# Kernel optimization log

Measured on AMD Instinct MI355X. Metric: run time of the kernel, lower is better.

Reference implementation:

```python
import jax, jax.numpy as jnp
import numpy as np

B, T, DMODEL = 2, 2048, 1024
H, DK, DV = 16, 64, 64
FF = 4096
EPS = 1e-5


def _layernorm_2d(x):
    # torch LayerNorm(normalized_shape=(T, dmodel)): normalize jointly over last two
    # dims, biased variance, weight=1 / bias=0 (freshly constructed each forward).
    mu = jnp.mean(x, axis=(1, 2), keepdims=True)
    var = jnp.mean((x - mu) ** 2, axis=(1, 2), keepdims=True)
    return (x - mu) / jnp.sqrt(var + EPS)


def setup_inputs() -> dict:
    key = jax.random.key(0)
    ks = jax.random.split(key, 9)
    s = 0.02  # small init for numerical sanity (original uses uniform(-1,1))
    return {
        "x": jax.random.normal(ks[0], (B, T, DMODEL), jnp.float32),
        "Wq": jax.random.normal(ks[1], (H, DMODEL, DK), jnp.float32) * s,
        "Wk": jax.random.normal(ks[2], (H, DMODEL, DK), jnp.float32) * s,
        "Wv": jax.random.normal(ks[3], (H, DMODEL, DV), jnp.float32) * s,
        "Wo": jax.random.normal(ks[4], (DMODEL, DMODEL), jnp.float32) * s,
        "W1": jax.random.normal(ks[5], (DMODEL, FF), jnp.float32) * s,
        "b1": jnp.zeros((FF,), jnp.float32),
        "W2": jax.random.normal(ks[6], (FF, DMODEL), jnp.float32) * s,
        "b2": jnp.zeros((DMODEL,), jnp.float32),
    }


def reference(x, Wq, Wk, Wv, Wo, W1, b1, W2, b2):
    b, t, d = x.shape
    h, _, dk = Wq.shape
    dv = Wv.shape[-1]
    # per-head projections: (B,H,T,dk/dv)
    Qp = jnp.einsum("btd,hdk->bhtk", x, Wq)
    Kp = jnp.einsum("btd,hdk->bhtk", x, Wk)
    Vp = jnp.einsum("btd,hdv->bhtv", x, Wv)
    scores = jnp.einsum("bhqk,bhsk->bhqs", Qp, Kp) / np.sqrt(dk).astype(np.float32)
    # NOTE: original does torch.softmax(heads, 2) -> softmax over the QUERY axis
    attn = jax.nn.softmax(scores, axis=2)
    heads = jnp.einsum("bhqs,bhsv->bqhv", attn, Vp).reshape(b, t, h * dv)
    att_out = heads @ Wo
    o1 = _layernorm_2d(x + att_out)
    ff = jnp.maximum(o1 @ W1 + b1, 0.0) @ W2 + b2
    return _layernorm_2d(o1 + ff)
```

## Files before the change

kernel.cpp:

```cpp
#include <hip/hip_runtime.h>
#include <hip/hip_bf16.h>
#include <cstddef>
#include <cstdint>

typedef __hip_bfloat16 hbf;
typedef __attribute__((ext_vector_type(8))) __bf16 bf16x8;
typedef __attribute__((ext_vector_type(4))) float f32x4;

#define B_ 2
#define T_ 2048
#define D_ 1024
#define H_ 16
#define FF_ 4096
#define EPS_ 1e-5f
#define SCALE_ 0.125f

__device__ __forceinline__ float bf2f(hbf v) { return __bfloat162float(v); }
__device__ __forceinline__ float ldin(const void* p, size_t i, int isbf) {
  return isbf ? __bfloat162float(((const hbf*)p)[i]) : ((const float*)p)[i];
}
__device__ __forceinline__ void ston(void* p, size_t i, float v, int isbf) {
  if (isbf) ((hbf*)p)[i] = __float2bfloat16(v);
  else ((float*)p)[i] = v;
}
__device__ __forceinline__ f32x4 mfma16(bf16x8 a, bf16x8 b, f32x4 c) {
  return __builtin_amdgcn_mfma_f32_16x16x32_bf16(a, b, c, 0, 0, 0);
}
__device__ __forceinline__ bf16x8 ldfrag(const hbf* p) {
  return *(const bf16x8*)p;
}
__device__ __forceinline__ void glds16(const hbf* g, hbf* l) {
  __builtin_amdgcn_global_load_lds(
      (const __attribute__((address_space(1))) void*)g,
      (__attribute__((address_space(3))) void*)l, 16, 0, 0);
}

__global__ __launch_bounds__(256) void detect_dtype(const unsigned* x,
                                                    int* flag) {
  __shared__ int cnt[256];
  int c = 0;
  for (int i = threadIdx.x; i < 4096; i += 256) {
    unsigned low = x[i] & 0xFFFFu;
    unsigned e = (low >> 7) & 0xFFu;
    if (e >= 100u && e <= 142u) c++;
  }
  cnt[threadIdx.x] = c;
  __syncthreads();
  for (int off = 128; off > 0; off >>= 1) {
    if ((int)threadIdx.x < off) cnt[threadIdx.x] += cnt[threadIdx.x + off];
    __syncthreads();
  }
  if (threadIdx.x == 0) *flag = (cnt[0] > 2458) ? 1 : 0;
}

__device__ __forceinline__ void tr_tile(const void* __restrict__ src,
                                        hbf* __restrict__ dst, int R, int C,
                                        size_t zoff, int cx, int ry, int f,
                                        float (*tile)[33]) {
  const int tx = threadIdx.x & 31, ty = threadIdx.x >> 5;
  const int c0 = cx * 32, r0 = ry * 32;
#pragma unroll
  for (int p = 0; p < 4; p++) {
    int rr = p * 8 + ty;
    tile[rr][tx] = ldin(src, zoff + (size_t)(r0 + rr) * C + c0 + tx, f);
  }
  __syncthreads();
#pragma unroll
  for (int p = 0; p < 4; p++) {
    int cc = p * 8 + ty;
    dst[zoff + (size_t)(c0 + cc) * R + r0 + tx] = __float2bfloat16(tile[tx][cc]);
  }
}

__global__ __launch_bounds__(256) void preconv(
    const void* __restrict__ x, const void* __restrict__ Wq,
    const void* __restrict__ Wk, const void* __restrict__ Wv,
    const void* __restrict__ Wo, const void* __restrict__ W1,
    const void* __restrict__ W2, const void* __restrict__ b1,
    const void* __restrict__ b2, hbf* __restrict__ xb,
    hbf* __restrict__ wqkvt, hbf* __restrict__ wot, hbf* __restrict__ w1t,
    hbf* __restrict__ w2t, hbf* __restrict__ b1b, hbf* __restrict__ b2b,
    const int* __restrict__ flag) {
  __shared__ float tile[32][33];
  const int f = *flag;
  const int bid = blockIdx.x;
  if (bid < 3072) {
    int which = bid >> 10;
    int r = bid & 1023;
    int z = r >> 6, rem = r & 63;
    int ry = rem >> 1, cx = rem & 1;
    const void* src = (which == 0) ? Wq : (which == 1) ? Wk : Wv;
    hbf* dst = wqkvt + (size_t)which * (D_ * D_);
    tr_tile(src, dst, 1024, 64, (size_t)z * 65536, cx, ry, f, tile);
  } else if (bid < 4096) {
    int t = bid - 3072;
    tr_tile(Wo, wot, 1024, 1024, 0, t & 31, t >> 5, f, tile);
  } else if (bid < 8192) {
    int t = bid - 4096;
    tr_tile(W1, w1t, 1024, 4096, 0, t & 127, t >> 7, f, tile);
  } else if (bid < 12288) {
    int t = bid - 8192;
    tr_tile(W2, w2t, 4096, 1024, 0, t & 31, t >> 5, f, tile);
  } else if (bid < 13312) {
    size_t base = (size_t)(bid - 12288) * 4096;
    for (int i = threadIdx.x; i < 4096; i += 256)
      xb[base + i] = __float2bfloat16(ldin(x, base + i, f));
  } else if (bid == 13312) {
    for (int i = threadIdx.x; i < FF_; i += 256)
      b1b[i] = __float2bfloat16(ldin(b1, i, f));
  } else {
    for (int i = threadIdx.x; i < D_; i += 256)
      b2b[i] = __float2bfloat16(ldin(b2, i, f));
  }
}

template <int MODE, int BM, int BN>
__global__ __launch_bounds__(256) void gemm_bt(
    const hbf* __restrict__ A, const hbf* __restrict__ Bt, hbf* __restrict__ C,
    float* __restrict__ Cf0, float* __restrict__ Cf1,
    const hbf* __restrict__ e1, float* __restrict__ red, int M, int N, int K,
    int LDK) {
  constexpr int WM = BM / 2, WN = BN / 2;
  constexpr int IF = WM / 16, JF = WN / 16;
  __shared__ alignas(16) hbf As[BM * 64];
  __shared__ alignas(16) hbf Bs[BN * 64];
  const int tid = threadIdx.x;
  const int wave = tid >> 6, lane = tid & 63;
  const int quad = lane >> 4, l16 = lane & 15;
  const int m0 = blockIdx.y * BM, n0 = blockIdx.x * BN;
  const int mw = (wave >> 1) * WM, nw = (wave & 1) * WN;
  const int srow = tid >> 3;
  const int scol = (tid & 7) * 8;
  const int kbase = (MODE == 4) ? blockIdx.z * K : 0;
  const f32x4 zero = {0.f, 0.f, 0.f, 0.f};
  f32x4 acc[IF][JF];
#pragma unroll
  for (int i = 0; i < IF; i++)
#pragma unroll
    for (int j = 0; j < JF; j++) acc[i][j] = zero;

  const hbf* ga = &A[(size_t)(m0 + srow) * LDK + kbase + scol];
  const hbf* gb = &Bt[(size_t)(n0 + srow) * LDK + kbase + scol];
  hbf* lA = &As[wave * 512];
  hbf* lB = &Bs[wave * 512];

  for (int k0 = 0; k0 < K; k0 += 64) {
#pragma unroll
    for (int c = 0; c < BM / 32; c++)
      glds16(ga + (size_t)(c * 32) * LDK + k0, lA + c * 2048);
#pragma unroll
    for (int c = 0; c < BN / 32; c++)
      glds16(gb + (size_t)(c * 32) * LDK + k0, lB + c * 2048);
    __syncthreads();
    bf16x8 af[2][IF], bfr[2][JF];
#pragma unroll
    for (int h = 0; h < 2; h++) {
#pragma unroll
      for (int i = 0; i < IF; i++)
        af[h][i] = ldfrag(&As[(mw + i * 16 + l16) * 64 + h * 32 + quad * 8]);
#pragma unroll
      for (int j = 0; j < JF; j++)
        bfr[h][j] = ldfrag(&Bs[(nw + j * 16 + l16) * 64 + h * 32 + quad * 8]);
    }
#pragma unroll
    for (int h = 0; h < 2; h++)
#pragma unroll
      for (int i = 0; i < IF; i++)
#pragma unroll
        for (int j = 0; j < JF; j++)
          acc[i][j] = mfma16(af[h][i], bfr[h][j], acc[i][j]);
    __syncthreads();
  }
  float ssum = 0.f, ssq = 0.f;
#pragma unroll
  for (int i = 0; i < IF; i++)
#pragma unroll
    for (int j = 0; j < JF; j++)
#pragma unroll
      for (int r = 0; r < 4; r++) {
        int m = m0 + mw + i * 16 + quad * 4 + r;
        int n = n0 + nw + j * 16 + l16;
        float v = acc[i][j][r];
        if (MODE == 0) {
          int which = n >> 10, n1 = n & 1023;
          int h = n1 >> 6, cc = n1 & 63;
          int b = m >> 11, t = m & (T_ - 1);
          if (which == 0) v *= SCALE_;
          C[(size_t)which * ((size_t)B_ * H_ * T_ * 64) +
            (((size_t)(b * H_ + h)) * T_ + t) * 64 + cc] = __float2bfloat16(v);
        } else if (MODE == 1) {
          hbf hv = __float2bfloat16(v + bf2f(e1[(size_t)m * N + n]));
          C[(size_t)m * N + n] = hv;
          float fv = bf2f(hv);
          ssum += fv;
          ssq += fv * fv;
        } else if (MODE == 2) {
          C[(size_t)m * N + n] = __float2bfloat16(fmaxf(v + bf2f(e1[n]), 0.f));
        } else if (MODE == 4) {
          float* Cf = blockIdx.z ? Cf1 : Cf0;
          Cf[(size_t)m * N + n] = v;
        }
      }
  if (MODE == 1) {
    float* sc = (float*)As;
    sc[tid] = ssum;
    sc[256 + tid] = ssq;
    __syncthreads();
    for (int off = 128; off > 0; off >>= 1) {
      if (tid < off) {
        sc[tid] += sc[tid + off];
        sc[256 + tid] += sc[256 + tid + off];
      }
      __syncthreads();
    }
    if (tid == 0) {
      int b = m0 >> 11;
      atomicAdd(&red[b * 2 + 0], sc[0]);
      atomicAdd(&red[b * 2 + 1], sc[256]);
    }
  }
}

__global__ __launch_bounds__(256) void attn_stats(const hbf* __restrict__ Q,
                                                  const hbf* __restrict__ K,
                                                  const hbf* __restrict__ V,
                                                  hbf* __restrict__ Vt) {
  __shared__ alignas(16) hbf Ks[64 * 72];
  __shared__ alignas(16) hbf Qs[64 * 72];
  __shared__ float sAdj[64];
  const int bh = blockIdx.y;
  const int s0 = blockIdx.x * 64;
  const int tid = threadIdx.x;
  const int wave = tid >> 6, lane = tid & 63;
  const int quad = lane >> 4, l16 = lane & 15;
  const int sw = wave * 16;
  const hbf* Kb = K + (size_t)bh * T_ * 64;
  const hbf* Qb = Q + (size_t)bh * T_ * 64;
  const hbf* Vb = V + (size_t)bh * T_ * 64;
  hbf* Vtb = Vt + (size_t)bh * 64 * T_;
  const int r_ = tid >> 3, c_ = (tid & 7) * 8;
#pragma unroll
  for (int c = 0; c < 2; c++) {
    int row = c * 32 + r_;
    *(float4*)(&Ks[row * 72 + c_]) =
        *(const float4*)(&Kb[(size_t)(s0 + row) * 64 + c_]);
  }
  __syncthreads();
  bf16x8 kf0 = ldfrag(&Ks[(sw + l16) * 72 + quad * 8]);
  bf16x8 kf1 = ldfrag(&Ks[(sw + l16) * 72 + 32 + quad * 8]);
  float m_thr[4], l_thr[4];
#pragma unroll
  for (int r = 0; r < 4; r++) {
    m_thr[r] = -1e30f;
    l_thr[r] = 0.f;
  }
  const f32x4 zero = {0.f, 0.f, 0.f, 0.f};
  for (int qt = 0; qt < T_ / 64; qt++) {
    if (qt) __syncthreads();
#pragma unroll
    for (int c = 0; c < 2; c++) {
      int row = c * 32 + r_;
      *(float4*)(&Qs[row * 72 + c_]) =
          *(const float4*)(&Qb[(size_t)(qt * 64 + row) * 64 + c_]);
    }
    __syncthreads();
    f32x4 acc[4];
#pragma unroll
    for (int j = 0; j < 4; j++) {
      bf16x8 qf0 = ldfrag(&Qs[(j * 16 + l16) * 72 + quad * 8]);
      bf16x8 qf1 = ldfrag(&Qs[(j * 16 + l16) * 72 + 32 + quad * 8]);
      f32x4 a = zero;
      a = mfma16(kf0, qf0, a);
      a = mfma16(kf1, qf1, a);
      acc[j] = a;
    }
#pragma unroll
    for (int r = 0; r < 4; r++) {
      float mt = fmaxf(fmaxf(acc[0][r], acc[1][r]),
                       fmaxf(acc[2][r], acc[3][r]));
      float nm = fmaxf(m_thr[r], mt);
      float s = l_thr[r] * __expf(m_thr[r] - nm);
#pragma unroll
      for (int j = 0; j < 4; j++) s += __expf(acc[j][r] - nm);
      l_thr[r] = s;
      m_thr[r] = nm;
    }
  }
#pragma unroll
  for (int d = 1; d < 16; d <<= 1) {
#pragma unroll
    for (int r = 0; r < 4; r++) {
      float om = __shfl_xor(m_thr[r], d);
      float ol = __shfl_xor(l_thr[r], d);
      float nm = fmaxf(m_thr[r], om);
      l_thr[r] = l_thr[r] * __expf(m_thr[r] - nm) + ol * __expf(om - nm);
      m_thr[r] = nm;
    }
  }
  if (l16 == 0) {
#pragma unroll
    for (int r = 0; r < 4; r++)
      sAdj[sw + quad * 4 + r] = m_thr[r] + __logf(l_thr[r]);
  }
  __syncthreads();
#pragma unroll
  for (int c = 0; c < 2; c++) {
    int e = (c * 256 + tid) * 8;
    int r = e >> 6, col = e & 63;
    union alignas(16) {
      hbf h[8];
      float4 f4;
    } u;
    u.f4 = *(const float4*)(&Vb[(size_t)(s0 + r) * 64 + col]);
    float sc = __expf(-sAdj[r]);
#pragma unroll
    for (int k2 = 0; k2 < 8; k2++)
      u.h[k2] = __float2bfloat16(bf2f(u.h[k2]) * sc);
    *(float4*)(&Ks[r * 72 + col]) = u.f4;
  }
  __syncthreads();
#pragma unroll
  for (int c = 0; c < 2; c++) {
    int e = (c * 256 + tid) * 8;
    int v = e >> 6, tt = e & 63;
    union alignas(16) {
      hbf h[8];
      float4 f4;
    } u;
#pragma unroll
    for (int k2 = 0; k2 < 8; k2++) u.h[k2] = Ks[(tt + k2) * 72 + v];
    *(float4*)(&Vtb[(size_t)v * T_ + s0 + tt]) = u.f4;
  }
}

__global__ __launch_bounds__(256) void attn_apply(const hbf* __restrict__ Q,
                                                  const hbf* __restrict__ K,
                                                  const hbf* __restrict__ Vt,
                                                  hbf* __restrict__ heads) {
  __shared__ alignas(16) hbf Ks[64 * 72];
  __shared__ alignas(16) hbf Vs[64 * 72];
  __shared__ alignas(16) hbf Ps[4 * 32 * 72];
  const int bh = blockIdx.y;
  const int b = bh >> 4, h = bh & 15;
  const int q0 = blockIdx.x * 128;
  const int tid = threadIdx.x;
  const int wave = tid >> 6, lane = tid & 63;
  const int quad = lane >> 4, l16 = lane & 15;
  const int qw = wave * 32;
  const hbf* Qb = Q + (size_t)bh * T_ * 64;
  const hbf* Kb = K + (size_t)bh * T_ * 64;
  const hbf* Vtb = Vt + (size_t)bh * 64 * T_;
  hbf* Pw = &Ps[wave * 32 * 72];
  const int r_ = tid >> 3, c_ = (tid & 7) * 8;
  bf16x8 qf[2][2];
#pragma unroll
  for (int i = 0; i < 2; i++)
#pragma unroll
    for (int hh = 0; hh < 2; hh++)
      qf[i][hh] = *(const bf16x8*)&Qb[(size_t)(q0 + qw + i * 16 + l16) * 64 +
                                      hh * 32 + quad * 8];
  const f32x4 zero = {0.f, 0.f, 0.f, 0.f};
  f32x4 accO[2][4];
#pragma unroll
  for (int i = 0; i < 2; i++)
#pragma unroll
    for (int j = 0; j < 4; j++) accO[i][j] = zero;

  for (int st = 0; st < T_ / 64; st++) {
    if (st) __syncthreads();
#pragma unroll
    for (int c = 0; c < 2; c++) {
      int row = c * 32 + r_;
      *(float4*)(&Ks[row * 72 + c_]) =
          *(const float4*)(&Kb[(size_t)(st * 64 + row) * 64 + c_]);
      *(float4*)(&Vs[row * 72 + c_]) =
          *(const float4*)(&Vtb[(size_t)row * T_ + st * 64 + c_]);
    }
    __syncthreads();
    f32x4 accS[2][4];
#pragma unroll
    for (int j = 0; j < 4; j++) {
      bf16x8 kf0 = ldfrag(&Ks[(j * 16 + l16) * 72 + quad * 8]);
      bf16x8 kf1 = ldfrag(&Ks[(j * 16 + l16) * 72 + 32 + quad * 8]);
#pragma unroll
      for (int i = 0; i < 2; i++) {
        f32x4 a = zero;
        a = mfma16(qf[i][0], kf0, a);
        a = mfma16(qf[i][1], kf1, a);
        accS[i][j] = a;
      }
    }
#pragma unroll
    for (int j = 0; j < 4; j++) {
#pragma unroll
      for (int i = 0; i < 2; i++)
#pragma unroll
        for (int r = 0; r < 4; r++) {
          float p = __expf(accS[i][j][r]);
          Pw[(i * 16 + quad * 4 + r) * 72 + j * 16 + l16] =
              __float2bfloat16(p);
        }
    }
    bf16x8 pf[2][2];
#pragma unroll
    for (int i = 0; i < 2; i++) {
      pf[i][0] = ldfrag(&Pw[(i * 16 + l16) * 72 + quad * 8]);
      pf[i][1] = ldfrag(&Pw[(i * 16 + l16) * 72 + 32 + quad * 8]);
    }
#pragma unroll
    for (int j2 = 0; j2 < 4; j2++) {
      bf16x8 vf0 = ldfrag(&Vs[(j2 * 16 + l16) * 72 + quad * 8]);
      bf16x8 vf1 = ldfrag(&Vs[(j2 * 16 + l16) * 72 + 32 + quad * 8]);
#pragma unroll
      for (int i = 0; i < 2; i++) {
        accO[i][j2] = mfma16(pf[i][0], vf0, accO[i][j2]);
        accO[i][j2] = mfma16(pf[i][1], vf1, accO[i][j2]);
      }
    }
  }
#pragma unroll
  for (int i = 0; i < 2; i++)
#pragma unroll
    for (int j2 = 0; j2 < 4; j2++)
#pragma unroll
      for (int r = 0; r < 4; r++) {
        int q = q0 + qw + i * 16 + quad * 4 + r;
        int v = j2 * 16 + l16;
        heads[((size_t)(b * T_ + q)) * D_ + h * 64 + v] =
            __float2bfloat16(accO[i][j2][r]);
      }
}

__global__ __launch_bounds__(256) void ln_norm(const hbf* __restrict__ src,
                                               const float* __restrict__ red,
                                               void* dst,
                                               const int* __restrict__ flag,
                                               int force_bf) {
  const int isbf = force_bf ? 1 : *flag;
  const float invN = 1.f / (float)(T_ * D_);
  for (size_t i = (size_t)blockIdx.x * 256 + threadIdx.x;
       i < (size_t)B_ * T_ * D_; i += (size_t)gridDim.x * 256) {
    int b = (int)(i >> 21);
    float mu = red[b * 2 + 0] * invN;
    float var = red[b * 2 + 1] * invN - mu * mu;
    ston(dst, i, (bf2f(src[i]) - mu) * rsqrtf(var + EPS_), isbf);
  }
}

__global__ __launch_bounds__(256) void ln2_stats(const float* __restrict__ P0,
                                                 const float* __restrict__ P1,
                                                 const hbf* __restrict__ o1,
                                                 const hbf* __restrict__ b2b,
                                                 float* __restrict__ red) {
  __shared__ float s1[256], s2[256];
  const int b = blockIdx.y;
  const size_t base = (size_t)b * (T_ * D_);
  float sum = 0.f, sq = 0.f;
  for (size_t i = (size_t)blockIdx.x * 256 + threadIdx.x; i < (size_t)T_ * D_;
       i += (size_t)gridDim.x * 256) {
    size_t e = base + i;
    float v = P0[e] + P1[e] + bf2f(b2b[i & (D_ - 1)]) + bf2f(o1[e]);
    sum += v;
    sq += v * v;
  }
  s1[threadIdx.x] = sum;
  s2[threadIdx.x] = sq;
  __syncthreads();
  for (int off = 128; off > 0; off >>= 1) {
    if ((int)threadIdx.x < off) {
      s1[threadIdx.x] += s1[threadIdx.x + off];
      s2[threadIdx.x] += s2[threadIdx.x + off];
    }
    __syncthreads();
  }
  if (threadIdx.x == 0) {
    atomicAdd(&red[b * 2 + 0], s1[0]);
    atomicAdd(&red[b * 2 + 1], s2[0]);
  }
}

__global__ __launch_bounds__(256) void ln2_norm(
    const float* __restrict__ P0, const float* __restrict__ P1,
    const hbf* __restrict__ o1, const hbf* __restrict__ b2b,
    const float* __restrict__ red, void* dst, const int* __restrict__ flag) {
  const int isbf = *flag;
  const float invN = 1.f / (float)(T_ * D_);
  for (size_t i = (size_t)blockIdx.x * 256 + threadIdx.x;
       i < (size_t)B_ * T_ * D_; i += (size_t)gridDim.x * 256) {
    int b = (int)(i >> 21);
    float mu = red[b * 2 + 0] * invN;
    float var = red[b * 2 + 1] * invN - mu * mu;
    float v = P0[i] + P1[i] + bf2f(b2b[i & (D_ - 1)]) + bf2f(o1[i]);
    ston(dst, i, (v - mu) * rsqrtf(var + EPS_), isbf);
  }
}

extern "C" void kernel_launch(void* const* d_in, const int* in_sizes, int n_in,
                              void* d_out, int out_size, void* d_ws,
                              size_t ws_size, hipStream_t stream) {
  const void* x = d_in[0];
  const void* Wq = d_in[1];
  const void* Wk = d_in[2];
  const void* Wv = d_in[3];
  const void* Wo = d_in[4];
  const void* W1 = d_in[5];
  const void* W2 = d_in[7];
  const void* b1 = d_in[6];
  const void* b2 = d_in[8];

  const size_t MB = 1024 * 1024;
  if (ws_size < 89 * MB) return;

  char* w = (char*)d_ws;
  hbf* xb = (hbf*)(w + 0 * MB);
  hbf* wqkvt = (hbf*)(w + 8 * MB);
  hbf* wot = (hbf*)(w + 14 * MB);
  hbf* w1t = (hbf*)(w + 16 * MB);
  hbf* w2t = (hbf*)(w + 24 * MB);
  hbf* Qb = (hbf*)(w + 32 * MB);
  hbf* Kb = (hbf*)(w + 40 * MB);
  hbf* Vb = (hbf*)(w + 48 * MB);
  hbf* Vtb = (hbf*)(w + 56 * MB);
  hbf* heads = (hbf*)(w + 64 * MB);
  hbf* r1 = (hbf*)(w + 72 * MB);
  hbf* o1 = (hbf*)(w + 80 * MB);
  hbf* ff1 = (hbf*)(w + 32 * MB);
  float* P0 = (float*)(w + 0 * MB);
  float* P1 = (float*)(w + 64 * MB);
  hbf* b1b = (hbf*)(w + 88 * MB);
  hbf* b2b = b1b + FF_;
  float* red = (float*)(b2b + D_);
  int* flag = (int*)(red + 8);

  hipMemsetAsync(red, 0, 8 * sizeof(float) + sizeof(int), stream);
  detect_dtype<<<1, 256, 0, stream>>>((const unsigned*)x, flag);

  const int M = B_ * T_;
  preconv<<<13314, 256, 0, stream>>>(x, Wq, Wk, Wv, Wo, W1, W2, b1, b2, xb,
                                     wqkvt, wot, w1t, w2t, b1b, b2b, flag);
  gemm_bt<0, 128, 128><<<dim3(24, 32), 256, 0, stream>>>(
      xb, wqkvt, Qb, nullptr, nullptr, nullptr, nullptr, M, 3 * D_, D_, D_);
  attn_stats<<<dim3(32, 32), 256, 0, stream>>>(Qb, Kb, Vb, Vtb);
  attn_apply<<<dim3(16, 32), 256, 0, stream>>>(Qb, Kb, Vtb, heads);
  gemm_bt<1, 128, 64><<<dim3(16, 32), 256, 0, stream>>>(
      heads, wot, r1, nullptr, nullptr, xb, red, M, D_, D_, D_);
  ln_norm<<<4096, 256, 0, stream>>>(r1, red, o1, flag, 1);
  gemm_bt<2, 128, 128><<<dim3(32, 32), 256, 0, stream>>>(
      o1, w1t, ff1, nullptr, nullptr, b1b, nullptr, M, FF_, D_, D_);
  gemm_bt<4, 128, 128><<<dim3(8, 32, 2), 256, 0, stream>>>(
      ff1, w2t, nullptr, P0, P1, nullptr, nullptr, M, D_, FF_ / 2, FF_);
  ln2_stats<<<dim3(256, B_), 256, 0, stream>>>(P0, P1, o1, b2b, red + 4);
  ln2_norm<<<2048, 256, 0, stream>>>(P0, P1, o1, b2b, red + 4, d_out, flag);
}
```

Before: 475.7 us.

## Fold LayerNorm1 into FFN1 GEMM, drop max tracking in softmax, prefetch attention tiles

Removes the ln_norm kernel. LayerNorm1 is folded into the W1 GEMM epilogue through the identity (x-mu)*rs@W1 = (x@W1 - mu*colsum(W1))*rs, with W1 column sums precomputed in preconv, and LN2 recomputes o1 from r1. The attention softmax drops the running-max rescaling: Q is pre-scaled by log2(e)/8 and raw exp2 is used, which assumes scores are small enough not to overflow. Attention kernels also prefetch the next Q or K/V tile into registers, and the memset is merged into detect_dtype. The changes trade numerical robustness and extra W1 reads for fewer passes and launches.

After: 611.4 us. 1.29x slower.

```diff
diff --git a/kernel.cpp b/kernel.cpp
--- a/kernel.cpp
+++ b/kernel.cpp
@@ -13,7 +13,7 @@
 #define H_ 16
 #define FF_ 4096
 #define EPS_ 1e-5f
-#define SCALE_ 0.125f
+#define QSCALE_ 0.18033688f
 
 __device__ __forceinline__ float bf2f(hbf v) { return __bfloat162float(v); }
 __device__ __forceinline__ float ldin(const void* p, size_t i, int isbf) {
@@ -28,6 +28,15 @@
 }
 __device__ __forceinline__ bf16x8 ldfrag(const hbf* p) {
   return *(const bf16x8*)p;
+}
+__device__ __forceinline__ float fexp2(float x) {
+#if __has_builtin(__builtin_amdgcn_exp2f)
+  return __builtin_amdgcn_exp2f(x);
+#else
+  float r;
+  asm("v_exp_f32 %0, %1" : "=v"(r) : "v"(x));
+  return r;
+#endif
 }
 __device__ __forceinline__ void glds16(const hbf* g, hbf* l) {
   __builtin_amdgcn_global_load_lds(
@@ -36,8 +45,9 @@
 }
 
 __global__ __launch_bounds__(256) void detect_dtype(const unsigned* x,
-                                                    int* flag) {
+                                                    int* flag, float* red) {
   __shared__ int cnt[256];
+  if (threadIdx.x < 8) red[threadIdx.x] = 0.f;
   int c = 0;
   for (int i = threadIdx.x; i < 4096; i += 256) {
     unsigned low = x[i] & 0xFFFFu;
@@ -80,7 +90,7 @@
     const void* __restrict__ b2, hbf* __restrict__ xb,
     hbf* __restrict__ wqkvt, hbf* __restrict__ wot, hbf* __restrict__ w1t,
     hbf* __restrict__ w2t, hbf* __restrict__ b1b, hbf* __restrict__ b2b,
-    const int* __restrict__ flag) {
+    float* __restrict__ sW1, const int* __restrict__ flag) {
   __shared__ float tile[32][33];
   const int f = *flag;
   const int bid = blockIdx.x;
@@ -108,18 +118,23 @@
   } else if (bid == 13312) {
     for (int i = threadIdx.x; i < FF_; i += 256)
       b1b[i] = __float2bfloat16(ldin(b1, i, f));
-  } else {
+  } else if (bid == 13313) {
     for (int i = threadIdx.x; i < D_; i += 256)
       b2b[i] = __float2bfloat16(ldin(b2, i, f));
+  } else {
+    int n = (bid - 13314) * 256 + threadIdx.x;
+    float s = 0.f;
+    for (int k = 0; k < D_; k++) s += ldin(W1, (size_t)k * FF_ + n, f);
+    sW1[n] = s;
   }
 }
 
 template <int MODE, int BM, int BN>
 __global__ __launch_bounds__(256) void gemm_bt(
     const hbf* __restrict__ A, const hbf* __restrict__ Bt, hbf* __restrict__ C,
-    float* __restrict__ Cf0, float* __restrict__ Cf1,
-    const hbf* __restrict__ e1, float* __restrict__ red, int M, int N, int K,
-    int LDK) {
+    float* __restrict__ Cf0, float* __restrict__ Cf1, float* __restrict__ Cf2,
+    const hbf* __restrict__ e1, float* __restrict__ red,
+    const float* __restrict__ sW1, int M, int N, int K, int LDK) {
   constexpr int WM = BM / 2, WN = BN / 2;
   constexpr int IF = WM / 16, JF = WN / 16;
   __shared__ alignas(16) hbf As[BM * 64];
@@ -171,6 +186,14 @@
           acc[i][j] = mfma16(af[h][i], bfr[h][j], acc[i][j]);
     __syncthreads();
   }
+  float mu = 0.f, rs = 0.f;
+  if (MODE == 5) {
+    const float invN = 1.f / (float)(T_ * D_);
+    int b = m0 >> 11;
+    mu = red[b * 2 + 0] * invN;
+    float var = red[b * 2 + 1] * invN - mu * mu;
+    rs = rsqrtf(var + EPS_);
+  }
   float ssum = 0.f, ssq = 0.f;
 #pragma unroll
   for (int i = 0; i < IF; i++)
@@ -185,7 +208,7 @@
           int which = n >> 10, n1 = n & 1023;
           int h = n1 >> 6, cc = n1 & 63;
           int b = m >> 11, t = m & (T_ - 1);
-          if (which == 0) v *= SCALE_;
+          if (which == 0) v *= QSCALE_;
           C[(size_t)which * ((size_t)B_ * H_ * T_ * 64) +
             (((size_t)(b * H_ + h)) * T_ + t) * 64 + cc] = __float2bfloat16(v);
         } else if (MODE == 1) {
@@ -194,11 +217,16 @@
           float fv = bf2f(hv);
           ssum += fv;
           ssq += fv * fv;
-        } else if (MODE == 2) {
-          C[(size_t)m * N + n] = __float2bfloat16(fmaxf(v + bf2f(e1[n]), 0.f));
         } else if (MODE == 4) {
-          float* Cf = blockIdx.z ? Cf1 : Cf0;
-          Cf[(size_t)m * N + n] = v;
+          if (blockIdx.z == 0) {
+            Cf0[(size_t)m * N + n] = v;
+          } else {
+            float* Cf = (m >> 11) ? Cf2 : Cf1;
+            Cf[(size_t)(m & 2047) * N + n] = v;
+          }
+        } else if (MODE == 5) {
+          float o = (v - mu * sW1[n]) * rs + bf2f(e1[n]);
+          C[(size_t)m * N + n] = __float2bfloat16(fmaxf(o, 0.f));
         }
       }
   if (MODE == 1) {
@@ -227,7 +255,7 @@
                                                   hbf* __restrict__ Vt) {
   __shared__ alignas(16) hbf Ks[64 * 72];
   __shared__ alignas(16) hbf Qs[64 * 72];
-  __shared__ float sAdj[64];
+  __shared__ float sSc[64];
   const int bh = blockIdx.y;
   const int s0 = blockIdx.x * 64;
   const int tid = threadIdx.x;
@@ -245,25 +273,27 @@
     *(float4*)(&Ks[row * 72 + c_]) =
         *(const float4*)(&Kb[(size_t)(s0 + row) * 64 + c_]);
   }
+  float4 qreg[2];
+#pragma unroll
+  for (int c = 0; c < 2; c++)
+    qreg[c] = *(const float4*)(&Qb[(size_t)(c * 32 + r_) * 64 + c_]);
   __syncthreads();
   bf16x8 kf0 = ldfrag(&Ks[(sw + l16) * 72 + quad * 8]);
   bf16x8 kf1 = ldfrag(&Ks[(sw + l16) * 72 + 32 + quad * 8]);
-  float m_thr[4], l_thr[4];
-#pragma unroll
-  for (int r = 0; r < 4; r++) {
-    m_thr[r] = -1e30f;
-    l_thr[r] = 0.f;
-  }
+  float l_thr[4] = {0.f, 0.f, 0.f, 0.f};
   const f32x4 zero = {0.f, 0.f, 0.f, 0.f};
   for (int qt = 0; qt < T_ / 64; qt++) {
-    if (qt) __syncthreads();
-#pragma unroll
-    for (int c = 0; c < 2; c++) {
-      int row = c * 32 + r_;
-      *(float4*)(&Qs[row * 72 + c_]) =
-          *(const float4*)(&Qb[(size_t)(qt * 64 + row) * 64 + c_]);
-    }
-    __syncthreads();
+#pragma unroll
+    for (int c = 0; c < 2; c++)
+      *(float4*)(&Qs[(c * 32 + r_) * 72 + c_]) = qreg[c];
+    __syncthreads();
+    if (qt + 1 < T_ / 64) {
+#pragma unroll
+      for (int c = 0; c < 2; c++)
+        qreg[c] = *(const float4*)(&Qb[(size_t)((qt + 1) * 64 + c * 32 + r_) *
+                                           64 +
+                                       c_]);
+    }
     f32x4 acc[4];
 #pragma unroll
     for (int j = 0; j < 4; j++) {
@@ -275,32 +305,18 @@
       acc[j] = a;
     }
 #pragma unroll
-    for (int r = 0; r < 4; r++) {
-      float mt = fmaxf(fmaxf(acc[0][r], acc[1][r]),
-                       fmaxf(acc[2][r], acc[3][r]));
-      float nm = fmaxf(m_thr[r], mt);
-      float s = l_thr[r] * __expf(m_thr[r] - nm);
-#pragma unroll
-      for (int j = 0; j < 4; j++) s += __expf(acc[j][r] - nm);
-      l_thr[r] = s;
-      m_thr[r] = nm;
-    }
-  }
-#pragma unroll
-  for (int d = 1; d < 16; d <<= 1) {
-#pragma unroll
-    for (int r = 0; r < 4; r++) {
-      float om = __shfl_xor(m_thr[r], d);
-      float ol = __shfl_xor(l_thr[r], d);
-      float nm = fmaxf(m_thr[r], om);
-      l_thr[r] = l_thr[r] * __expf(m_thr[r] - nm) + ol * __expf(om - nm);
-      m_thr[r] = nm;
-    }
-  }
+    for (int r = 0; r < 4; r++)
+#pragma unroll
+      for (int j = 0; j < 4; j++) l_thr[r] += fexp2(acc[j][r]);
+    __syncthreads();
+  }
+#pragma unroll
+  for (int d = 1; d < 16; d <<= 1)
+#pragma unroll
+    for (int r = 0; r < 4; r++) l_thr[r] += __shfl_xor(l_thr[r], d);
   if (l16 == 0) {
 #pragma unroll
-    for (int r = 0; r < 4; r++)
-      sAdj[sw + quad * 4 + r] = m_thr[r] + __logf(l_thr[r]);
+    for (int r = 0; r < 4; r++) sSc[sw + quad * 4 + r] = 1.f / l_thr[r];
   }
   __syncthreads();
 #pragma unroll
@@ -312,7 +328,7 @@
       float4 f4;
     } u;
     u.f4 = *(const float4*)(&Vb[(size_t)(s0 + r) * 64 + col]);
-    float sc = __expf(-sAdj[r]);
+    float sc = sSc[r];
 #pragma unroll
     for (int k2 = 0; k2 < 8; k2++)
       u.h[k2] = __float2bfloat16(bf2f(u.h[k2]) * sc);
@@ -366,17 +382,31 @@
 #pragma unroll
     for (int j = 0; j < 4; j++) accO[i][j] = zero;
 
+  float4 kreg[2], vreg[2];
+#pragma unroll
+  for (int c = 0; c < 2; c++) {
+    int row = c * 32 + r_;
+    kreg[c] = *(const float4*)(&Kb[(size_t)row * 64 + c_]);
+    vreg[c] = *(const float4*)(&Vtb[(size_t)row * T_ + c_]);
+  }
   for (int st = 0; st < T_ / 64; st++) {
-    if (st) __syncthreads();
 #pragma unroll
     for (int c = 0; c < 2; c++) {
       int row = c * 32 + r_;
-      *(float4*)(&Ks[row * 72 + c_]) =
-          *(const float4*)(&Kb[(size_t)(st * 64 + row) * 64 + c_]);
-      *(float4*)(&Vs[row * 72 + c_]) =
-          *(const float4*)(&Vtb[(size_t)row * T_ + st * 64 + c_]);
-    }
-    __syncthreads();
+      *(float4*)(&Ks[row * 72 + c_]) = kreg[c];
+      *(float4*)(&Vs[row * 72 + c_]) = vreg[c];
+    }
+    __syncthreads();
+    if (st + 1 < T_ / 64) {
+#pragma unroll
+      for (int c = 0; c < 2; c++) {
+        int row = c * 32 + r_;
+        kreg[c] =
+            *(const float4*)(&Kb[(size_t)((st + 1) * 64 + row) * 64 + c_]);
+        vreg[c] =
+            *(const float4*)(&Vtb[(size_t)row * T_ + (st + 1) * 64 + c_]);
+      }
+    }
     f32x4 accS[2][4];
 #pragma unroll
     for (int j = 0; j < 4; j++) {
@@ -396,9 +426,8 @@
       for (int i = 0; i < 2; i++)
 #pragma unroll
         for (int r = 0; r < 4; r++) {
-          float p = __expf(accS[i][j][r]);
           Pw[(i * 16 + quad * 4 + r) * 72 + j * 16 + l16] =
-              __float2bfloat16(p);
+              __float2bfloat16(fexp2(accS[i][j][r]));
         }
     }
     bf16x8 pf[2][2];
@@ -417,6 +446,7 @@
         accO[i][j2] = mfma16(pf[i][1], vf1, accO[i][j2]);
       }
     }
+    __syncthreads();
   }
 #pragma unroll
   for (int i = 0; i < 2; i++)
@@ -431,35 +461,23 @@
       }
 }
 
-__global__ __launch_bounds__(256) void ln_norm(const hbf* __restrict__ src,
-                                               const float* __restrict__ red,
-                                               void* dst,
-                                               const int* __restrict__ flag,
-                                               int force_bf) {
-  const int isbf = force_bf ? 1 : *flag;
-  const float invN = 1.f / (float)(T_ * D_);
-  for (size_t i = (size_t)blockIdx.x * 256 + threadIdx.x;
-       i < (size_t)B_ * T_ * D_; i += (size_t)gridDim.x * 256) {
-    int b = (int)(i >> 21);
-    float mu = red[b * 2 + 0] * invN;
-    float var = red[b * 2 + 1] * invN - mu * mu;
-    ston(dst, i, (bf2f(src[i]) - mu) * rsqrtf(var + EPS_), isbf);
-  }
-}
-
-__global__ __launch_bounds__(256) void ln2_stats(const float* __restrict__ P0,
-                                                 const float* __restrict__ P1,
-                                                 const hbf* __restrict__ o1,
-                                                 const hbf* __restrict__ b2b,
-                                                 float* __restrict__ red) {
+__global__ __launch_bounds__(256) void ln2_stats(
+    const float* __restrict__ P0, const float* __restrict__ P1a,
+    const float* __restrict__ P1b, const hbf* __restrict__ r1,
+    const hbf* __restrict__ b2b, float* __restrict__ red) {
   __shared__ float s1[256], s2[256];
   const int b = blockIdx.y;
   const size_t base = (size_t)b * (T_ * D_);
+  const float invN = 1.f / (float)(T_ * D_);
+  const float mu1 = red[b * 2 + 0] * invN;
+  const float var1 = red[b * 2 + 1] * invN - mu1 * mu1;
+  const float rs1 = rsqrtf(var1 + EPS_);
+  const float* P1 = b ? P1b : P1a;
   float sum = 0.f, sq = 0.f;
   for (size_t i = (size_t)blockIdx.x * 256 + threadIdx.x; i < (size_t)T_ * D_;
        i += (size_t)gridDim.x * 256) {
-    size_t e = base + i;
-    float v = P0[e] + P1[e] + bf2f(b2b[i & (D_ - 1)]) + bf2f(o1[e]);
+    float v = P0[base + i] + P1[i] + bf2f(b2b[i & (D_ - 1)]) +
+              (bf2f(r1[base + i]) - mu1) * rs1;
     sum += v;
     sq += v * v;
   }
@@ -474,24 +492,32 @@
     __syncthreads();
   }
   if (threadIdx.x == 0) {
-    atomicAdd(&red[b * 2 + 0], s1[0]);
-    atomicAdd(&red[b * 2 + 1], s2[0]);
+    atomicAdd(&red[4 + b * 2 + 0], s1[0]);
+    atomicAdd(&red[4 + b * 2 + 1], s2[0]);
   }
 }
 
 __global__ __launch_bounds__(256) void ln2_norm(
-    const float* __restrict__ P0, const float* __restrict__ P1,
-    const hbf* __restrict__ o1, const hbf* __restrict__ b2b,
-    const float* __restrict__ red, void* dst, const int* __restrict__ flag) {
+    const float* __restrict__ P0, const float* __restrict__ P1a,
+    const float* __restrict__ P1b, const hbf* __restrict__ r1,
+    const hbf* __restrict__ b2b, const float* __restrict__ red, void* dst,
+    const int* __restrict__ flag) {
   const int isbf = *flag;
+  const int b = blockIdx.y;
+  const size_t base = (size_t)b * (T_ * D_);
   const float invN = 1.f / (float)(T_ * D_);
-  for (size_t i = (size_t)blockIdx.x * 256 + threadIdx.x;
-       i < (size_t)B_ * T_ * D_; i += (size_t)gridDim.x * 256) {
-    int b = (int)(i >> 21);
-    float mu = red[b * 2 + 0] * invN;
-    float var = red[b * 2 + 1] * invN - mu * mu;
-    float v = P0[i] + P1[i] + bf2f(b2b[i & (D_ - 1)]) + bf2f(o1[i]);
-    ston(dst, i, (v - mu) * rsqrtf(var + EPS_), isbf);
+  const float mu1 = red[b * 2 + 0] * invN;
+  const float var1 = red[b * 2 + 1] * invN - mu1 * mu1;
+  const float rs1 = rsqrtf(var1 + EPS_);
+  const float mu2 = red[4 + b * 2 + 0] * invN;
+  const float var2 = red[4 + b * 2 + 1] * invN - mu2 * mu2;
+  const float rs2 = rsqrtf(var2 + EPS_);
+  const float* P1 = b ? P1b : P1a;
+  for (size_t i = (size_t)blockIdx.x * 256 + threadIdx.x; i < (size_t)T_ * D_;
+       i += (size_t)gridDim.x * 256) {
+    float v = P0[base + i] + P1[i] + bf2f(b2b[i & (D_ - 1)]) +
+              (bf2f(r1[base + i]) - mu1) * rs1;
+    ston(dst, base + i, (v - mu2) * rs2, isbf);
   }
 }
 
@@ -523,32 +549,36 @@
   hbf* Vtb = (hbf*)(w + 56 * MB);
   hbf* heads = (hbf*)(w + 64 * MB);
   hbf* r1 = (hbf*)(w + 72 * MB);
-  hbf* o1 = (hbf*)(w + 80 * MB);
   hbf* ff1 = (hbf*)(w + 32 * MB);
   float* P0 = (float*)(w + 0 * MB);
-  float* P1 = (float*)(w + 64 * MB);
+  float* P1a = (float*)(w + 64 * MB);
+  float* P1b = (float*)(w + 80 * MB);
   hbf* b1b = (hbf*)(w + 88 * MB);
   hbf* b2b = b1b + FF_;
   float* red = (float*)(b2b + D_);
   int* flag = (int*)(red + 8);
-
-  hipMemsetAsync(red, 0, 8 * sizeof(float) + sizeof(int), stream);
-  detect_dtype<<<1, 256, 0, stream>>>((const unsigned*)x, flag);
+  float* sW1 = (float*)(flag + 1);
+
+  detect_dtype<<<1, 256, 0, stream>>>((const unsigned*)x, flag, red);
 
   const int M = B_ * T_;
-  preconv<<<13314, 256, 0, stream>>>(x, Wq, Wk, Wv, Wo, W1, W2, b1, b2, xb,
-                                     wqkvt, wot, w1t, w2t, b1b, b2b, flag);
+  preconv<<<13330, 256, 0, stream>>>(x, Wq, Wk, Wv, Wo, W1, W2, b1, b2, xb,
+                                     wqkvt, wot, w1t, w2t, b1b, b2b, sW1,
+                                     flag);
   gemm_bt<0, 128, 128><<<dim3(24, 32), 256, 0, stream>>>(
-      xb, wqkvt, Qb, nullptr, nullptr, nullptr, nullptr, M, 3 * D_, D_, D_);
+      xb, wqkvt, Qb, nullptr, nullptr, nullptr, nullptr, nullptr, nullptr, M,
+      3 * D_, D_, D_);
   attn_stats<<<dim3(32, 32), 256, 0, stream>>>(Qb, Kb, Vb, Vtb);
   attn_apply<<<dim3(16, 32), 256, 0, stream>>>(Qb, Kb, Vtb, heads);
   gemm_bt<1, 128, 64><<<dim3(16, 32), 256, 0, stream>>>(
-      heads, wot, r1, nullptr, nullptr, xb, red, M, D_, D_, D_);
-  ln_norm<<<4096, 256, 0, stream>>>(r1, red, o1, flag, 1);
-  gemm_bt<2, 128, 128><<<dim3(32, 32), 256, 0, stream>>>(
-      o1, w1t, ff1, nullptr, nullptr, b1b, nullptr, M, FF_, D_, D_);
+      heads, wot, r1, nullptr, nullptr, nullptr, xb, red, nullptr, M, D_, D_,
+      D_);
+  gemm_bt<5, 128, 128><<<dim3(32, 32), 256, 0, stream>>>(
+      r1, w1t, ff1, nullptr, nullptr, nullptr, b1b, red, sW1, M, FF_, D_, D_);
   gemm_bt<4, 128, 128><<<dim3(8, 32, 2), 256, 0, stream>>>(
-      ff1, w2t, nullptr, P0, P1, nullptr, nullptr, M, D_, FF_ / 2, FF_);
-  ln2_stats<<<dim3(256, B_), 256, 0, stream>>>(P0, P1, o1, b2b, red + 4);
-  ln2_norm<<<2048, 256, 0, stream>>>(P0, P1, o1, b2b, red + 4, d_out, flag);
-}
+      ff1, w2t, nullptr, P0, P1a, P1b, nullptr, nullptr, nullptr, M, D_,
+      FF_ / 2, FF_);
+  ln2_stats<<<dim3(256, B_), 256, 0, stream>>>(P0, P1a, P1b, r1, b2b, red);
+  ln2_norm<<<dim3(1024, B_), 256, 0, stream>>>(P0, P1a, P1b, r1, b2b, red,
+                                               d_out, flag);
+}
```
